# Kernel optimization log

Hardware: AMD Instinct MI355X
Metric: run time of the kernel (lower is better)

Reference implementation:

```python
import jax, jax.numpy as jnp
import numpy as np

NUM_ITERATIONS = 3


def _squash(s):
    # s: [B, J, S]. Faithful to the torch code: squash norm is computed over
    # dim=2 of s_j [B,1,J,S,1], i.e. the num_unit (J) axis here.
    mag_sq = jnp.sum(s * s, axis=1, keepdims=True)  # [B, 1, S]
    mag = jnp.sqrt(mag_sq)
    return s * (mag_sq / (1.0 + mag_sq) / mag)


def setup_inputs() -> dict:
    key = jax.random.key(0)
    k1, k2 = jax.random.split(key)
    B, U, C, J, S = 128, 8, 2048, 32, 16
    x = jax.random.normal(k1, (B, U, C), dtype=jnp.float32)
    W = jax.random.normal(k2, (1, C, J, S, U), dtype=jnp.float32)
    return {"x": x, "W": W}


def reference(x, W):
    # x: [B, in_unit, in_channel]; W: [1, C, J, S, U]
    xt = jnp.swapaxes(x, 1, 2)          # [B, C, U]
    Wc = W[0]                           # [C, J, S, U]
    # u_hat = W @ x (per input capsule c, output capsule j): [B, C, J, S]
    u_hat = jnp.einsum('cjsu,bcu->bcjs', Wc, xt)
    B, C, J, _ = u_hat.shape
    b = jnp.zeros((C, J), dtype=u_hat.dtype)
    v = None
    for _ in range(NUM_ITERATIONS):
        # legacy F.softmax on 4D [1,C,J,1] defaults to dim=1 -> over C
        c = jax.nn.softmax(b, axis=0)                      # [C, J]
        s = jnp.einsum('cj,bcjs->bjs', c, u_hat)           # [B, J, S]
        v = _squash(s)                                     # [B, J, S]
        # agreement, mean over batch (keepdim handled by shape [C,J])
        b = b + jnp.einsum('bcjs,bjs->cj', u_hat, v) / B
    return v[..., None]  # [B, num_unit, unit_size, 1] == v_j.squeeze(1)
```

## Files before the change

kernel.cpp:

```cpp
#include <hip/hip_runtime.h>
#include <hip/hip_bf16.h>

#define BB 128
#define UU 8
#define CC 2048
#define JJ 32
#define SS 16

typedef unsigned int u32;
typedef unsigned short u16;
typedef __attribute__((ext_vector_type(8))) short bf16x8;
typedef __attribute__((ext_vector_type(4))) float f32x4;

__device__ __forceinline__ float bflo(u32 p) { return __uint_as_float(p << 16); }
__device__ __forceinline__ float bfhi(u32 p) { return __uint_as_float(p & 0xffff0000u); }
__device__ __forceinline__ u32 f2b(float f) {
    u32 bits = __float_as_uint(f);
    u32 r = bits + 0x7fffu + ((bits >> 16) & 1u);
    return r >> 16;
}
__device__ __forceinline__ u32 pack2(float a, float b) { return f2b(a) | (f2b(b) << 16); }
__device__ __forceinline__ uint4 scale4(uint4 p, float cw) {
    uint4 o;
    o.x = pack2(bflo(p.x) * cw, bfhi(p.x) * cw);
    o.y = pack2(bflo(p.y) * cw, bfhi(p.y) * cw);
    o.z = pack2(bflo(p.z) * cw, bfhi(p.z) * cw);
    o.w = pack2(bflo(p.w) * cw, bfhi(p.w) * cw);
    return o;
}

__global__ __launch_bounds__(256) void k_prep(const float* __restrict__ x,
                                              const float* __restrict__ W,
                                              u16* __restrict__ xA,
                                              u16* __restrict__ xB,
                                              u16* __restrict__ Wn,
                                              float* __restrict__ bbp) {
    __shared__ uint4 ldsu[16][129];
    int blk = blockIdx.x, t = threadIdx.x;
    if (blk < 1024) {
        int b = blk >> 3;
        int c = (blk & 7) * 256 + t;
        const float* xf = x + (size_t)b * UU * CC;
        float v[8];
#pragma unroll
        for (int u = 0; u < 8; ++u) v[u] = xf[u * CC + c];
        uint4 p;
        p.x = pack2(v[0], v[1]);
        p.y = pack2(v[2], v[3]);
        p.z = pack2(v[4], v[5]);
        p.w = pack2(v[6], v[7]);
        ((uint4*)xA)[(size_t)b * CC + c] = p;
    } else if (blk < 2048) {
        int bb2 = blk - 1024;
        int u = bb2 >> 7, c0 = (bb2 & 127) * 16;
        float* ldsf = (float*)ldsu;
        int b = t >> 1, h = t & 1;
        const float4* x4 = (const float4*)(x + ((size_t)b * UU + u) * CC + c0);
        float4 lo = x4[h * 2], hi = x4[h * 2 + 1];
        ldsf[(h * 8 + 0) * 129 + b] = lo.x; ldsf[(h * 8 + 1) * 129 + b] = lo.y;
        ldsf[(h * 8 + 2) * 129 + b] = lo.z; ldsf[(h * 8 + 3) * 129 + b] = lo.w;
        ldsf[(h * 8 + 4) * 129 + b] = hi.x; ldsf[(h * 8 + 5) * 129 + b] = hi.y;
        ldsf[(h * 8 + 6) * 129 + b] = hi.z; ldsf[(h * 8 + 7) * 129 + b] = hi.w;
        __syncthreads();
        int ci = t >> 4, k8 = t & 15;
        const float* r = ldsf + ci * 129 + k8 * 8;
        uint4 p;
        p.x = pack2(r[0], r[1]);
        p.y = pack2(r[2], r[3]);
        p.z = pack2(r[4], r[5]);
        p.w = pack2(r[6], r[7]);
        ((uint4*)xB)[((size_t)u * CC + c0 + ci) * 16 + k8] = p;
    } else if (blk < 2560) {
        int bb2 = blk - 2048;
        int ct = bb2 & 127, nt = bb2 >> 7;
        int c0 = ct * 16, n0 = nt * 128;
        const float4* Wf = (const float4*)W;
        for (int q = t; q < 2048; q += 256) {
            int ci = q >> 7, ni = q & 127;
            size_t widx = (size_t)(c0 + ci) * 512 + n0 + ni;
            float4 lo = Wf[2 * widx], hi = Wf[2 * widx + 1];
            uint4 o;
            o.x = pack2(lo.x, lo.y);
            o.y = pack2(lo.z, lo.w);
            o.z = pack2(hi.x, hi.y);
            o.w = pack2(hi.z, hi.w);
            ldsu[ci][ni] = o;
        }
        __syncthreads();
        for (int q = t; q < 2048; q += 256) {
            int ni = q >> 4, ci = q & 15;
            ((uint4*)Wn)[(size_t)(n0 + ni) * 2048 + c0 + ci] = ldsu[ci][ni];
        }
    } else {
        int base = (blk - 2560) * 4096 + t;
#pragma unroll
        for (int r = 0; r < 16; ++r) bbp[base + r * 256] = 0.f;
    }
}

__global__ __launch_bounds__(256) void k_softmax(const float* __restrict__ bbp,
                                                 float* __restrict__ ccp) {
    int j = blockIdx.x, t = threadIdx.x;
    __shared__ float red[4];
    __shared__ float bcast[2];
    const float* row = bbp + j * CC;
    float m = -1e30f;
    for (int c = t; c < CC; c += 256) m = fmaxf(m, row[c]);
#pragma unroll
    for (int o = 32; o > 0; o >>= 1) m = fmaxf(m, __shfl_down(m, o, 64));
    if ((t & 63) == 0) red[t >> 6] = m;
    __syncthreads();
    if (t == 0) bcast[0] = fmaxf(fmaxf(red[0], red[1]), fmaxf(red[2], red[3]));
    __syncthreads();
    float mm = bcast[0];
    float ssum = 0.f;
    for (int c = t; c < CC; c += 256) ssum += expf(row[c] - mm);
#pragma unroll
    for (int o = 32; o > 0; o >>= 1) ssum += __shfl_down(ssum, o, 64);
    if ((t & 63) == 0) red[t >> 6] = ssum;
    __syncthreads();
    if (t == 0) bcast[1] = red[0] + red[1] + red[2] + red[3];
    __syncthreads();
    float inv = 1.0f / bcast[1];
    for (int c = t; c < CC; c += 256) ccp[j * CC + c] = expf(row[c] - mm) * inv;
}

__global__ __launch_bounds__(256) void k_gemmA(const u16* __restrict__ xA,
                                               const u16* __restrict__ Wn,
                                               const float* __restrict__ ccp,
                                               int use_cc,
                                               float* __restrict__ spart) {
    const bf16x8* A8 = (const bf16x8*)xA;
    const uint4* B4 = (const uint4*)Wn;
    int t = threadIdx.x;
    int w = t >> 6, lane = t & 63;
    int gw = blockIdx.x * 4 + w;
    int sl = gw >> 6, rest = gw & 63;
    int mg = rest & 3, ng = rest >> 2;
    int ln = lane & 15, quad = lane >> 4;
    int rowA0 = (mg * 32 + ln) * 2048;
    int rowA1 = rowA0 + 16 * 2048;
    int rowB0 = (ng * 32 + ln) * 2048;
    int rowB1 = rowB0 + 16 * 2048;
    const float* cc0 = ccp + (2 * ng) * CC;
    const float* cc1 = cc0 + CC;
    int kk = sl * 64 + quad;
    f32x4 acc00 = {0.f, 0.f, 0.f, 0.f};
    f32x4 acc01 = acc00, acc10 = acc00, acc11 = acc00;
#pragma unroll 4
    for (int step = 0; step < 16; ++step) {
        bf16x8 a0 = A8[rowA0 + kk];
        bf16x8 a1 = A8[rowA1 + kk];
        uint4 wb0 = B4[rowB0 + kk];
        uint4 wb1 = B4[rowB1 + kk];
        if (use_cc) {
            float cw0 = cc0[kk];
            float cw1 = cc1[kk];
            wb0 = scale4(wb0, cw0);
            wb1 = scale4(wb1, cw1);
        }
        bf16x8 b0 = __builtin_bit_cast(bf16x8, wb0);
        bf16x8 b1 = __builtin_bit_cast(bf16x8, wb1);
        kk += 4;
        acc00 = __builtin_amdgcn_mfma_f32_16x16x32_bf16(a0, b0, acc00, 0, 0, 0);
        acc01 = __builtin_amdgcn_mfma_f32_16x16x32_bf16(a0, b1, acc01, 0, 0, 0);
        acc10 = __builtin_amdgcn_mfma_f32_16x16x32_bf16(a1, b0, acc10, 0, 0, 0);
        acc11 = __builtin_amdgcn_mfma_f32_16x16x32_bf16(a1, b1, acc11, 0, 0, 0);
    }
    float* outp = spart + sl * (BB * JJ * SS);
    int b0r = mg * 32 + quad * 4;
    int n00 = ng * 32 + ln;
#pragma unroll
    for (int r = 0; r < 4; ++r) {
        int b = b0r + r;
        outp[b * 512 + n00] = acc00[r];
        outp[b * 512 + n00 + 16] = acc01[r];
        outp[(b + 16) * 512 + n00] = acc10[r];
        outp[(b + 16) * 512 + n00 + 16] = acc11[r];
    }
}

__global__ __launch_bounds__(512) void k_rsq(const float* __restrict__ spart,
                                             u16* __restrict__ vB,
                                             float* __restrict__ out,
                                             float scale_pre, int write_out) {
    __shared__ float s[512];
    __shared__ float sc[16];
    int b = blockIdx.x, n = threadIdx.x;
    float v = 0.f;
#pragma unroll
    for (int sl = 0; sl < 32; ++sl) v += spart[sl * (BB * JJ * SS) + b * 512 + n];
    v *= scale_pre;
    s[n] = v;
    __syncthreads();
    if (n < 16) {
        float msq = 0.f;
#pragma unroll
        for (int jj = 0; jj < 32; ++jj) {
            float tv = s[jj * 16 + n];
            msq = fmaf(tv, tv, msq);
        }
        sc[n] = msq / ((1.f + msq) * sqrtf(fmaxf(msq, 1e-30f)));
    }
    __syncthreads();
    float vv = s[n] * sc[n & 15];
    vB[n * BB + b] = (u16)f2b(vv);
    if (write_out) out[b * 512 + n] = vv;
}

__global__ __launch_bounds__(256) void k_gemmBf(const u16* __restrict__ vB,
                                                const u16* __restrict__ xB,
                                                const u16* __restrict__ Wn,
                                                float* __restrict__ bbp) {
    const bf16x8* A8 = (const bf16x8*)vB;
    const bf16x8* B8 = (const bf16x8*)xB;
    const uint4* Wn4 = (const uint4*)Wn;
    int t = threadIdx.x;
    int w = t >> 6, lane = t & 63;
    int gw = blockIdx.x * 4 + w;
    int u = gw >> 10, rest = gw & 1023;
    int nt = rest & 15, c0 = (rest >> 4) * 32;
    int n0 = nt * 32;
    int ln = lane & 15, quad = lane >> 4;
    bf16x8 av[2][4], bx[2][4];
#pragma unroll
    for (int mt = 0; mt < 2; ++mt)
#pragma unroll
        for (int st = 0; st < 4; ++st)
            av[mt][st] = A8[(n0 + mt * 16 + ln) * 16 + quad + 4 * st];
#pragma unroll
    for (int ct = 0; ct < 2; ++ct)
#pragma unroll
        for (int st = 0; st < 4; ++st)
            bx[ct][st] = B8[((size_t)u * CC + c0 + ct * 16 + ln) * 16 + quad + 4 * st];
    f32x4 acc[2][2];
    acc[0][0] = {0.f, 0.f, 0.f, 0.f};
    acc[0][1] = acc[0][0]; acc[1][0] = acc[0][0]; acc[1][1] = acc[0][0];
#pragma unroll
    for (int st = 0; st < 4; ++st)
#pragma unroll
        for (int mt = 0; mt < 2; ++mt)
#pragma unroll
            for (int ct = 0; ct < 2; ++ct)
                acc[mt][ct] = __builtin_amdgcn_mfma_f32_16x16x32_bf16(
                    av[mt][st], bx[ct][st], acc[mt][ct], 0, 0, 0);
#pragma unroll
    for (int mt = 0; mt < 2; ++mt) {
        int j = 2 * nt + mt;
#pragma unroll
        for (int ct = 0; ct < 2; ++ct) {
            int c = c0 + ct * 16 + ln;
            float val = 0.f;
#pragma unroll
            for (int r = 0; r < 4; ++r) {
                int n = n0 + mt * 16 + quad * 4 + r;
                uint4 wp = Wn4[(size_t)n * 2048 + c];
                u32 warr[4] = {wp.x, wp.y, wp.z, wp.w};
                u32 ww = warr[u >> 1];
                float wv = (u & 1) ? bfhi(ww) : bflo(ww);
                val = fmaf(acc[mt][ct][r], wv, val);
            }
            val += __shfl_xor(val, 16, 64);
            val += __shfl_xor(val, 32, 64);
            if (quad == 0)
                atomicAdd(&bbp[j * CC + c], val * (1.0f / BB));
        }
    }
}

extern "C" void kernel_launch(void* const* d_in, const int* in_sizes, int n_in,
                              void* d_out, int out_size, void* d_ws, size_t ws_size,
                              hipStream_t stream) {
    const float* x = (const float*)d_in[0];
    const float* W = (const float*)d_in[1];
    if (in_sizes[0] == CC * JJ * SS * UU) {
        x = (const float*)d_in[1];
        W = (const float*)d_in[0];
    }
    float* out = (float*)d_out;

    char* ws = (char*)d_ws;
    u16* xA = (u16*)(ws + (16u << 20));
    u16* xB = (u16*)(ws + (20u << 20));
    u16* Wn = (u16*)(ws + (24u << 20));
    float* spart = (float*)(ws + (40u << 20));
    size_t b48 = (size_t)48u << 20;
    u16* vB = (u16*)(ws + b48);
    float* bbp = (float*)(ws + b48 + 131072);
    float* ccp = (float*)(ws + b48 + 393216);

    k_prep<<<2576, 256, 0, stream>>>(x, W, xA, xB, Wn, bbp);

    for (int it = 0; it < 3; ++it) {
        if (it > 0) k_softmax<<<32, 256, 0, stream>>>(bbp, ccp);
        k_gemmA<<<512, 256, 0, stream>>>(xA, Wn, ccp, it > 0 ? 1 : 0, spart);
        k_rsq<<<128, 512, 0, stream>>>(spart, vB, out,
                                       it == 0 ? (1.0f / 2048.0f) : 1.0f,
                                       it == 2 ? 1 : 0);
        if (it < 2) k_gemmBf<<<2048, 256, 0, stream>>>(vB, xB, Wn, bbp);
    }
}
```

Measured before the change: 212.8 us.

## Stage gemmA operands in LDS with 128x128 block tiles and 64 K-splits

k_gemmA now has each 512-thread block cooperatively load a 128-row A tile and a 128-column B tile (scaled by the routing coefficients) into shared memory. Each wave then computes a 64x32 output sub-tile from LDS instead of every wave fetching its own operands from global memory. This is meant to cut redundant global loads of x and W and to reuse each B scaling across waves. The K-split count rises from 32 to 64, which doubles the partial-sum buffer and the reduction work in k_rsq, and the buffer is moved to the start of the workspace to make room.

```diff
diff --git a/kernel.cpp b/kernel.cpp
--- a/kernel.cpp
+++ b/kernel.cpp
@@ -125,59 +125,75 @@
     for (int c = t; c < CC; c += 256) ccp[j * CC + c] = expf(row[c] - mm) * inv;
 }
 
-__global__ __launch_bounds__(256) void k_gemmA(const u16* __restrict__ xA,
+__global__ __launch_bounds__(512) void k_gemmA(const u16* __restrict__ xA,
                                                const u16* __restrict__ Wn,
                                                const float* __restrict__ ccp,
                                                int use_cc,
                                                float* __restrict__ spart) {
-    const bf16x8* A8 = (const bf16x8*)xA;
-    const uint4* B4 = (const uint4*)Wn;
+    __shared__ uint4 As[128][9];
+    __shared__ uint4 Bs[128][9];
+    const uint4* xA4 = (const uint4*)xA;
+    const uint4* Wn4 = (const uint4*)Wn;
     int t = threadIdx.x;
+    int sl = blockIdx.x >> 2;
+    int n0 = (blockIdx.x & 3) * 128;
     int w = t >> 6, lane = t & 63;
-    int gw = blockIdx.x * 4 + w;
-    int sl = gw >> 6, rest = gw & 63;
-    int mg = rest & 3, ng = rest >> 2;
+    int mh = w & 1, nq = w >> 1;
     int ln = lane & 15, quad = lane >> 4;
-    int rowA0 = (mg * 32 + ln) * 2048;
-    int rowA1 = rowA0 + 16 * 2048;
-    int rowB0 = (ng * 32 + ln) * 2048;
-    int rowB1 = rowB0 + 16 * 2048;
-    const float* cc0 = ccp + (2 * ng) * CC;
-    const float* cc1 = cc0 + CC;
-    int kk = sl * 64 + quad;
-    f32x4 acc00 = {0.f, 0.f, 0.f, 0.f};
-    f32x4 acc01 = acc00, acc10 = acc00, acc11 = acc00;
-#pragma unroll 4
-    for (int step = 0; step < 16; ++step) {
-        bf16x8 a0 = A8[rowA0 + kk];
-        bf16x8 a1 = A8[rowA1 + kk];
-        uint4 wb0 = B4[rowB0 + kk];
-        uint4 wb1 = B4[rowB1 + kk];
-        if (use_cc) {
-            float cw0 = cc0[kk];
-            float cw1 = cc1[kk];
-            wb0 = scale4(wb0, cw0);
-            wb1 = scale4(wb1, cw1);
-        }
-        bf16x8 b0 = __builtin_bit_cast(bf16x8, wb0);
-        bf16x8 b1 = __builtin_bit_cast(bf16x8, wb1);
-        kk += 4;
-        acc00 = __builtin_amdgcn_mfma_f32_16x16x32_bf16(a0, b0, acc00, 0, 0, 0);
-        acc01 = __builtin_amdgcn_mfma_f32_16x16x32_bf16(a0, b1, acc01, 0, 0, 0);
-        acc10 = __builtin_amdgcn_mfma_f32_16x16x32_bf16(a1, b0, acc10, 0, 0, 0);
-        acc11 = __builtin_amdgcn_mfma_f32_16x16x32_bf16(a1, b1, acc11, 0, 0, 0);
+    f32x4 acc[4][2];
+#pragma unroll
+    for (int mt = 0; mt < 4; ++mt)
+#pragma unroll
+        for (int nt2 = 0; nt2 < 2; ++nt2) acc[mt][nt2] = {0.f, 0.f, 0.f, 0.f};
+
+    for (int ch = 0; ch < 4; ++ch) {
+        int cbase = sl * 32 + ch * 8;
+#pragma unroll
+        for (int r2 = 0; r2 < 2; ++r2) {
+            int q = t + r2 * 512;
+            int row = q >> 3, k8 = q & 7;
+            As[row][k8] = xA4[(size_t)row * 2048 + cbase + k8];
+        }
+#pragma unroll
+        for (int r2 = 0; r2 < 2; ++r2) {
+            int q = t + r2 * 512;
+            int ni = q >> 3, k8 = q & 7;
+            uint4 wb = Wn4[(size_t)(n0 + ni) * 2048 + cbase + k8];
+            if (use_cc) wb = scale4(wb, ccp[((n0 + ni) >> 4) * CC + cbase + k8]);
+            Bs[ni][k8] = wb;
+        }
+        __syncthreads();
+#pragma unroll
+        for (int st = 0; st < 2; ++st) {
+            bf16x8 af[4], bf[2];
+#pragma unroll
+            for (int mt = 0; mt < 4; ++mt)
+                af[mt] = __builtin_bit_cast(bf16x8,
+                         As[mh * 64 + mt * 16 + ln][st * 4 + quad]);
+#pragma unroll
+            for (int nt2 = 0; nt2 < 2; ++nt2)
+                bf[nt2] = __builtin_bit_cast(bf16x8,
+                          Bs[nq * 32 + nt2 * 16 + ln][st * 4 + quad]);
+#pragma unroll
+            for (int mt = 0; mt < 4; ++mt)
+#pragma unroll
+                for (int nt2 = 0; nt2 < 2; ++nt2)
+                    acc[mt][nt2] = __builtin_amdgcn_mfma_f32_16x16x32_bf16(
+                        af[mt], bf[nt2], acc[mt][nt2], 0, 0, 0);
+        }
+        __syncthreads();
     }
     float* outp = spart + sl * (BB * JJ * SS);
-    int b0r = mg * 32 + quad * 4;
-    int n00 = ng * 32 + ln;
-#pragma unroll
-    for (int r = 0; r < 4; ++r) {
-        int b = b0r + r;
-        outp[b * 512 + n00] = acc00[r];
-        outp[b * 512 + n00 + 16] = acc01[r];
-        outp[(b + 16) * 512 + n00] = acc10[r];
-        outp[(b + 16) * 512 + n00 + 16] = acc11[r];
-    }
+#pragma unroll
+    for (int mt = 0; mt < 4; ++mt)
+#pragma unroll
+        for (int nt2 = 0; nt2 < 2; ++nt2)
+#pragma unroll
+            for (int r = 0; r < 4; ++r) {
+                int b = mh * 64 + mt * 16 + quad * 4 + r;
+                int n = n0 + nq * 32 + nt2 * 16 + ln;
+                outp[b * 512 + n] = acc[mt][nt2][r];
+            }
 }
 
 __global__ __launch_bounds__(512) void k_rsq(const float* __restrict__ spart,
@@ -189,7 +205,7 @@
     int b = blockIdx.x, n = threadIdx.x;
     float v = 0.f;
 #pragma unroll
-    for (int sl = 0; sl < 32; ++sl) v += spart[sl * (BB * JJ * SS) + b * 512 + n];
+    for (int sl = 0; sl < 64; ++sl) v += spart[sl * (BB * JJ * SS) + b * 512 + n];
     v *= scale_pre;
     s[n] = v;
     __syncthreads();
@@ -280,10 +296,10 @@
     float* out = (float*)d_out;
 
     char* ws = (char*)d_ws;
+    float* spart = (float*)ws;
     u16* xA = (u16*)(ws + (16u << 20));
     u16* xB = (u16*)(ws + (20u << 20));
     u16* Wn = (u16*)(ws + (24u << 20));
-    float* spart = (float*)(ws + (40u << 20));
     size_t b48 = (size_t)48u << 20;
     u16* vB = (u16*)(ws + b48);
     float* bbp = (float*)(ws + b48 + 131072);
@@ -293,7 +309,7 @@
 
     for (int it = 0; it < 3; ++it) {
         if (it > 0) k_softmax<<<32, 256, 0, stream>>>(bbp, ccp);
-        k_gemmA<<<512, 256, 0, stream>>>(xA, Wn, ccp, it > 0 ? 1 : 0, spart);
+        k_gemmA<<<256, 512, 0, stream>>>(xA, Wn, ccp, it > 0 ? 1 : 0, spart);
         k_rsq<<<128, 512, 0, stream>>>(spart, vB, out,
                                        it == 0 ? (1.0f / 2048.0f) : 1.0f,
                                        it == 2 ? 1 : 0);
```

Measured after the change: 235.7 us. 1.11x slower.
